# Kernel tuning notes

Measured on AMD Instinct MI355X. Metric: run time of the kernel, lower is better.

## Reference

```python
import jax, jax.numpy as jnp
import numpy as np

BN_EPS = 1e-5
INTERP_EPS = 1e-8


def setup_inputs() -> dict:
    key = jax.random.key(0)
    ks = jax.random.split(key, 8)
    B, N, S, D1, D2 = 8, 8192, 2048, 128, 256
    C_in, C_mid, C_out = D1 + D2, 256, 256
    return {
        "xyz1": jax.random.normal(ks[0], (B, 3, N), dtype=jnp.float32),
        "xyz2": jax.random.normal(ks[1], (B, 3, S), dtype=jnp.float32),
        "points1": jax.random.normal(ks[2], (B, D1, N), dtype=jnp.float32),
        "points2": jax.random.normal(ks[3], (B, D2, S), dtype=jnp.float32),
        "W0": jax.random.normal(ks[4], (C_mid, C_in), dtype=jnp.float32) * (1.0 / np.sqrt(C_in)),
        "b0": jnp.zeros((C_mid,), dtype=jnp.float32),
        "gamma0": jnp.ones((C_mid,), dtype=jnp.float32),
        "beta0": jnp.zeros((C_mid,), dtype=jnp.float32),
        "W1": jax.random.normal(ks[5], (C_out, C_mid), dtype=jnp.float32) * (1.0 / np.sqrt(C_mid)),
        "b1": jnp.zeros((C_out,), dtype=jnp.float32),
    }


def reference(xyz1, xyz2, points1, points2, W0, b0, gamma0, beta0, W1, b1):
    B, _, N = xyz1.shape
    S = xyz2.shape[2]
    x1 = jnp.transpose(xyz1, (0, 2, 1))  # (B, N, 3)
    x2 = jnpp = jnp.transpose(xyz2, (0, 2, 1))  # (B, S, 3)
    # squared distances: (B, N, S)
    d = (jnp.sum(x1 ** 2, -1)[:, :, None]
         + jnp.sum(x2 ** 2, -1)[:, None, :]
         - 2.0 * jnp.einsum('bnc,bsc->bns', x1, x2))
    # 3 nearest neighbors (fused top-3 instead of full sort; same math)
    neg_d, idx = jax.lax.top_k(-d, 3)  # (B, N, 3)
    dists = -neg_d
    recip = 1.0 / (dists + INTERP_EPS)
    weight = recip / jnp.sum(recip, axis=2, keepdims=True)  # (B, N, 3)
    p2t = jnp.transpose(points2, (0, 2, 1))  # (B, S, D2)
    D2 = p2t.shape[-1]
    gathered = jnp.take_along_axis(p2t, idx.reshape(B, N * 3, 1), axis=1).reshape(B, N, 3, D2)
    interp = jnp.einsum('bnkc,bnk->bcn', gathered, weight)  # (B, D2, N)
    new_points = jnp.concatenate([interp, points1], axis=1)  # (B, D2+D1, N)
    # conv0 (1x1) + BatchNorm (train mode, batch stats) + ReLU
    h = jnp.einsum('oc,bcn->bon', W0, new_points) + b0[None, :, None]
    mean = jnp.mean(h, axis=(0, 2), keepdims=True)
    var = jnp.mean((h - mean) ** 2, axis=(0, 2), keepdims=True)  # biased, as torch BN
    h = gamma0[None, :, None] * (h - mean) * jax.lax.rsqrt(var + BN_EPS) + beta0[None, :, None]
    h = jax.nn.relu(h)
    # conv1 (1x1) + Identity (module pairs conv1 with nn.Identity) + ReLU
    h = jnp.einsum('oc,bcn->bon', W1, h) + b1[None, :, None]
    return jax.nn.relu(h)
```

## Files before the change

### kernel.cpp

```cpp
#include <hip/hip_runtime.h>
#include <stdint.h>

constexpr int B = 8, N = 8192, S = 2048, D1 = 128, D2 = 256;
constexpr int CIN = 384, CMID = 256, COUT = 256;

typedef __attribute__((ext_vector_type(8))) _Float16 half8;
typedef __attribute__((ext_vector_type(4))) _Float16 half4;
typedef __attribute__((ext_vector_type(4))) float f32x4;

union HU { uint32_t u; _Float16 h[2]; };


__global__ __launch_bounds__(256) void k_prep(const float* __restrict__ xyz2,
                                              float* __restrict__ dout) {
  const int gid = blockIdx.x * 256 + threadIdx.x;
  const int b = gid >> 11, s = gid & 2047;
  const float* x2 = xyz2 + (size_t)b * 3 * S;
  const float sx = x2[s], sy = x2[s + S], sz = x2[s + 2 * S];
  float4 v = {sx, sy, sz, sx * sx + sy * sy + sz * sz};
  *(float4*)(dout + ((size_t)(b * 256 + 208)) * 8192 + (size_t)s * 4) = v;
}

__global__ __launch_bounds__(256) void k_top3(const float* __restrict__ xyz1,
                                              const float* __restrict__ dP4,
                                              uint32_t* __restrict__ pw3) {
  __shared__ float md[4][3][64];
  __shared__ int mi[4][3][64];
  __shared__ float snrm[64];
  const int tid = threadIdx.x;
  const int wv = tid >> 6, lane = tid & 63;
  const int b = blockIdx.y;
  const int n = blockIdx.x * 64 + lane;
  const float* x1 = xyz1 + (size_t)b * 3 * N;
  const float ax = x1[n], ay = x1[n + N], az = x1[n + 2 * N];
  const float* P4 = dP4 + ((size_t)(b * 256 + 208)) * 8192;
  if (wv == 0) snrm[lane] = ax * ax + ay * ay + az * az;

  const float nax = -2.f * ax, nay = -2.f * ay, naz = -2.f * az;
  float e0 = 1e30f, e1 = 1e30f, e2 = 1e30f;
  int j0 = 0, j1 = 0, j2 = 0;
  const int s0 = wv * (S / 4), s1 = s0 + (S / 4);
#pragma unroll 8
  for (int s = s0; s < s1; ++s) {
    const float4 v = *(const float4*)(P4 + (size_t)s * 4);
    const float d = fmaf(nax, v.x, fmaf(nay, v.y, fmaf(naz, v.z, v.w)));
    const bool c0 = d < e0, c1 = d < e1, c2 = d < e2;
    const int u2 = c1 ? j1 : s;
    const int u1 = c0 ? j0 : s;
    j2 = c2 ? u2 : j2;
    j1 = c1 ? u1 : j1;
    j0 = c0 ? s : j0;
    e2 = __builtin_amdgcn_fmed3f(e1, e2, d);
    e1 = __builtin_amdgcn_fmed3f(e0, e1, d);
    e0 = fminf(e0, d);
  }
  md[wv][0][lane] = e0; mi[wv][0][lane] = j0;
  md[wv][1][lane] = e1; mi[wv][1][lane] = j1;
  md[wv][2][lane] = e2; mi[wv][2][lane] = j2;
  __syncthreads();
  if (tid < 64) {
    float f0 = md[0][0][tid], f1 = md[0][1][tid], f2 = md[0][2][tid];
    int g0 = mi[0][0][tid], g1 = mi[0][1][tid], g2 = mi[0][2][tid];
#pragma unroll
    for (int w = 1; w < 4; ++w)
#pragma unroll
      for (int k = 0; k < 3; ++k) {
        float d = md[w][k][tid];
        int i = mi[w][k][tid];
        if (d < f2) {
          if (d < f1) {
            f2 = f1; g2 = g1;
            if (d < f0) { f1 = f0; g1 = g0; f0 = d; g0 = i; }
            else        { f1 = d;  g1 = i; }
          } else { f2 = d; g2 = i; }
        }
      }
    const float rn = snrm[tid];
    float q0 = fmaxf(f0 + rn, 0.f);
    float q1 = fmaxf(f1 + rn, 0.f);
    float q2 = fmaxf(f2 + rn, 0.f);
    float r0 = 1.0f / (q0 + 1e-8f), r1 = 1.0f / (q1 + 1e-8f), r2 = 1.0f / (q2 + 1e-8f);
    float inv = 1.0f / (r0 + r1 + r2);
    auto pack = [](int i, float w) -> uint32_t {
      uint32_t q = (uint32_t)(w * 2097152.0f + 0.5f);
      if (q > 0x1FFFFFu) q = 0x1FFFFFu;
      return ((uint32_t)i << 21) | q;
    };
    size_t base = ((size_t)b * N + blockIdx.x * 64 + tid) * 3;
    pw3[base]     = pack(g0, r0 * inv);
    pw3[base + 1] = pack(g1, r1 * inv);
    pw3[base + 2] = pack(g2, r2 * inv);
  }
}

__global__ __launch_bounds__(256) void k_G(const float* __restrict__ points2,
                                           const float* __restrict__ W0,
                                           float* __restrict__ dout) {
  __shared__ half8 A_lds[4][256];
  __shared__ half8 B_lds[4][32];
  __shared__ float CT[32][258];
  const int tid = threadIdx.x;
  const int b = blockIdx.x >> 6;
  const int s0 = (blockIdx.x & 63) * 32;
  f32x4 acc[4][2] = {};
  const int wv = tid >> 6, lane = tid & 63;
  const int ln = lane & 15, quad = lane >> 4;
  const int bn = tid & 31, bkc = tid >> 5;
  const int ar = tid >> 3, ac4 = tid & 7;

  for (int kk = 0; kk < 256; kk += 32) {
    __syncthreads();
#pragma unroll
    for (int p = 0; p < 8; ++p) {
      int row = ar + 32 * p;
      const float4 v = *(const float4*)(W0 + (size_t)row * CIN + kk + ac4 * 4);
      half4 hv = {(_Float16)v.x, (_Float16)v.y, (_Float16)v.z, (_Float16)v.w};
      *(half4*)((_Float16*)&A_lds[ac4 >> 1][row] + (ac4 & 1) * 4) = hv;
    }
    {
      half4 hv;
#pragma unroll
      for (int j = 0; j < 4; ++j)
        hv[j] = (_Float16)points2[((size_t)(b * 256 + kk + bkc * 4 + j)) * S + s0 + bn];
      *(half4*)((_Float16*)&B_lds[bkc >> 1][bn] + (bkc & 1) * 4) = hv;
    }
    __syncthreads();
    half8 af[4], bf[2];
#pragma unroll
    for (int i = 0; i < 4; ++i) af[i] = A_lds[quad][wv * 64 + i * 16 + ln];
#pragma unroll
    for (int j = 0; j < 2; ++j) bf[j] = B_lds[quad][j * 16 + ln];
#pragma unroll
    for (int i = 0; i < 4; ++i)
#pragma unroll
      for (int j = 0; j < 2; ++j)
        acc[i][j] = __builtin_amdgcn_mfma_f32_16x16x32_f16(af[i], bf[j], acc[i][j], 0, 0, 0);
  }
  __syncthreads();
#pragma unroll
  for (int i = 0; i < 4; ++i)
#pragma unroll
    for (int reg = 0; reg < 4; ++reg) {
      int row = wv * 64 + i * 16 + quad * 4 + reg;
#pragma unroll
      for (int j = 0; j < 2; ++j) CT[j * 16 + ln][row] = acc[i][j][reg];
    }
  __syncthreads();
  const int sl = tid >> 3, g = tid & 7;
  float* g0 = dout + ((size_t)(b * 256 + 128)) * 8192 + (size_t)(s0 + sl) * 256 + g * 32;
#pragma unroll
  for (int q = 0; q < 8; ++q)
    *(float4*)(g0 + q * 4) = *(const float4*)&CT[sl][g * 32 + q * 4];
}

__global__ __launch_bounds__(256) void k_interp(const uint32_t* __restrict__ pw3,
                                                const float* __restrict__ dout_c,
                                                uint32_t* __restrict__ dout_u) {
  __shared__ int sidx[96];
  __shared__ float sw[96];
  const int tid = threadIdx.x;
  const int b = blockIdx.x >> 8;
  const int n0 = (blockIdx.x & 255) * 32;
  if (tid < 96) {
    uint32_t p = pw3[((size_t)b * N + n0) * 3 + tid];
    sidx[tid] = (int)(p >> 21);
    sw[tid] = (float)(p & 0x1FFFFFu) * (1.0f / 2097152.0f);
  }
  __syncthreads();
  const int colL = tid >> 3, p = tid & 7;
  const float* Gb = dout_c + ((size_t)(b * 256 + 128)) * 8192;
  float a[32];
#pragma unroll
  for (int q = 0; q < 32; ++q) a[q] = 0.f;
#pragma unroll
  for (int k = 0; k < 3; ++k) {
    int j = sidx[colL * 3 + k];
    float w = sw[colL * 3 + k];
    const float* g = Gb + (size_t)j * 256 + p * 32;
#pragma unroll
    for (int q = 0; q < 8; ++q) {
      float4 v = *(const float4*)(g + q * 4);
      a[q * 4 + 0] += w * v.x; a[q * 4 + 1] += w * v.y;
      a[q * 4 + 2] += w * v.z; a[q * 4 + 3] += w * v.w;
    }
  }
#pragma unroll
  for (int q = 0; q < 16; ++q) {
    int cp = p * 16 + q;
    HU u;
    u.h[0] = (_Float16)a[2 * q];
    u.h[1] = (_Float16)a[2 * q + 1];
    dout_u[((size_t)(b * 256 + cp)) * 8192 + n0 + colL] = u.u;
  }
}

__global__ __launch_bounds__(256) void k_wpack(const float* __restrict__ W0,
                                               const float* __restrict__ W1,
                                               _Float16* __restrict__ W1h,
                                               _Float16* __restrict__ W0h) {
  const int bid = blockIdx.x;
  if (bid < 64) {
    const int gid = bid * 256 + threadIdx.x;
    const float4 v = *(const float4*)(W1 + (size_t)gid * 4);
    half4 h = {(_Float16)v.x, (_Float16)v.y, (_Float16)v.z, (_Float16)v.w};
    *(half4*)(W1h + (size_t)gid * 4) = h;
  } else {
    const int gid = (bid - 64) * 256 + threadIdx.x;
    const int row = gid >> 5, c4 = gid & 31;
    const float4 v = *(const float4*)(W0 + (size_t)row * CIN + 256 + c4 * 4);
    half4 h = {(_Float16)v.x, (_Float16)v.y, (_Float16)v.z, (_Float16)v.w};
    *(half4*)(W0h + (size_t)row * 128 + c4 * 4) = h;
  }
}

__global__ __launch_bounds__(256) void k_h(uint32_t* __restrict__ h2,
                                           float* __restrict__ dpart,
                                           const float* __restrict__ points1,
                                           const _Float16* __restrict__ W0h,
                                           const float* __restrict__ b0) {
  __shared__ half8 B_lds[16][32];
  __shared__ float red_s[256], red_q[256], sb0[256];
  const int tid = threadIdx.x;
  const int b = blockIdx.x >> 8;
  const int cb = blockIdx.x & 255;
  const int n0 = cb * 32;
  sb0[tid] = b0[tid];
  const int wv = tid >> 6, lane = tid & 63;
  const int ln = lane & 15, quad = lane >> 4;

  f32x4 acc[4][2];
#pragma unroll
  for (int i = 0; i < 4; ++i) {
    const int rb = wv * 64 + i * 16 + quad * 4;
    const int cp0 = rb >> 1;
#pragma unroll
    for (int j = 0; j < 2; ++j) {
      const int col = n0 + j * 16 + ln;
      const size_t a0 = ((size_t)(b * 256 + cp0)) * 8192 + col;
      HU ua, ub;
      ua.u = h2[a0];
      ub.u = h2[a0 + 8192];
      acc[i][j][0] = (float)ua.h[0];
      acc[i][j][1] = (float)ua.h[1];
      acc[i][j][2] = (float)ub.h[0];
      acc[i][j][3] = (float)ub.h[1];
    }
  }
  {
    const int col = tid & 31;
    const int kc0 = tid >> 5;
#pragma unroll
    for (int it = 0; it < 2; ++it) {
      const int kc = kc0 + 8 * it;
      half8 hv;
#pragma unroll
      for (int j = 0; j < 8; ++j)
        hv[j] = (_Float16)points1[((size_t)(b * D1 + kc * 8 + j)) * N + n0 + col];
      B_lds[kc][col] = hv;
    }
  }
  __syncthreads();
  for (int kk = 0; kk < 128; kk += 32) {
    half8 af[4], bf[2];
#pragma unroll
    for (int i = 0; i < 4; ++i) {
      const int row = wv * 64 + i * 16 + ln;
      af[i] = *(const half8*)(W0h + (size_t)row * 128 + kk + quad * 8);
    }
#pragma unroll
    for (int j = 0; j < 2; ++j)
      bf[j] = B_lds[(kk >> 3) + quad][j * 16 + ln];
#pragma unroll
    for (int i = 0; i < 4; ++i)
#pragma unroll
      for (int j = 0; j < 2; ++j)
        acc[i][j] = __builtin_amdgcn_mfma_f32_16x16x32_f16(af[i], bf[j], acc[i][j], 0, 0, 0);
  }
#pragma unroll
  for (int i = 0; i < 4; ++i) {
    const int rb = wv * 64 + i * 16 + quad * 4;
    const int cp0 = rb >> 1;
    float rs[4] = {0.f, 0.f, 0.f, 0.f}, rq[4] = {0.f, 0.f, 0.f, 0.f};
#pragma unroll
    for (int j = 0; j < 2; ++j) {
      const int col = n0 + j * 16 + ln;
      const size_t a0 = ((size_t)(b * 256 + cp0)) * 8192 + col;
      _Float16 e0 = (_Float16)(acc[i][j][0] + sb0[rb + 0]);
      _Float16 e1 = (_Float16)(acc[i][j][1] + sb0[rb + 1]);
      _Float16 e2 = (_Float16)(acc[i][j][2] + sb0[rb + 2]);
      _Float16 e3 = (_Float16)(acc[i][j][3] + sb0[rb + 3]);
      HU o0, o1;
      o0.h[0] = e0; o0.h[1] = e1; o1.h[0] = e2; o1.h[1] = e3;
      h2[a0] = o0.u;
      h2[a0 + 8192] = o1.u;
      float f0 = (float)e0, f1 = (float)e1, f2 = (float)e2, f3 = (float)e3;
      rs[0] += f0; rq[0] += f0 * f0;
      rs[1] += f1; rq[1] += f1 * f1;
      rs[2] += f2; rq[2] += f2 * f2;
      rs[3] += f3; rq[3] += f3 * f3;
    }
#pragma unroll
    for (int reg = 0; reg < 4; ++reg) {
      float s = rs[reg], q = rq[reg];
#pragma unroll
      for (int m = 1; m < 16; m <<= 1) {
        s += __shfl_xor(s, m);
        q += __shfl_xor(q, m);
      }
      if (ln == 0) { red_s[rb + reg] = s; red_q[rb + reg] = q; }
    }
  }
  __syncthreads();
  float* part = dpart + ((size_t)(b * 256 + 192)) * 8192 + (size_t)cb * 512;
  part[tid] = red_s[tid];
  part[256 + tid] = red_q[tid];
}

__global__ __launch_bounds__(256) void k_bn(const float* __restrict__ dpart,
                                            const float* __restrict__ gamma,
                                            const float* __restrict__ beta,
                                            float* __restrict__ bna,
                                            float* __restrict__ bnb) {
  const int c = blockIdx.x;
  const int tid = threadIdx.x;
  float s = 0.f, q = 0.f;
#pragma unroll
  for (int u = tid; u < 2048; u += 256) {
    int b = u >> 8, cb = u & 255;
    const float* part = dpart + ((size_t)(b * 256 + 192)) * 8192 + (size_t)cb * 512;
    s += part[c];
    q += part[256 + c];
  }
#pragma unroll
  for (int m = 1; m < 64; m <<= 1) {
    s += __shfl_xor(s, m);
    q += __shfl_xor(q, m);
  }
  __shared__ float ls[4], lq[4];
  if ((tid & 63) == 0) { ls[tid >> 6] = s; lq[tid >> 6] = q; }
  __syncthreads();
  if (tid == 0) {
    float st = ls[0] + ls[1] + ls[2] + ls[3];
    float qt = lq[0] + lq[1] + lq[2] + lq[3];
    const float invn = 1.0f / (float)(B * N);
    float mean = st * invn;
    float var = qt * invn - mean * mean;
    float a = gamma[c] * rsqrtf(var + 1e-5f);
    bna[c] = a;
    bnb[c] = beta[c] - mean * a;
  }
}

__global__ __launch_bounds__(256) void k_fused1(const uint32_t* h2,
                                                const _Float16* __restrict__ W1h,
                                                const float* __restrict__ b1,
                                                const float* __restrict__ bna,
                                                const float* __restrict__ bnb,
                                                float* out) {
  __shared__ uint32_t Hh[32 * 33 * 4];
  __shared__ float sa[256], sb[256], sb1[256];
  const int tid = threadIdx.x;
  const int b = blockIdx.x >> 8;
  const int n0 = (blockIdx.x & 255) * 32;
  sa[tid] = bna[tid]; sb[tid] = bnb[tid]; sb1[tid] = b1[tid];
  __syncthreads();
  {
    const int c4 = tid & 7;
    const int rg = tid >> 3;
#pragma unroll
    for (int q = 0; q < 4; ++q) {
      const int cp = rg + 32 * q;
      const uint4 v = *(const uint4*)&h2[((size_t)(b * 256 + cp)) * 8192 + n0 + c4 * 4];
      const int k0 = 2 * cp;
      const float a0 = sa[k0], a1 = sa[k0 + 1], b0v = sb[k0], b1v = sb[k0 + 1];
      const int kc = cp >> 2, sub = cp & 3;
      const uint32_t vv[4] = {v.x, v.y, v.z, v.w};
#pragma unroll
      for (int m = 0; m < 4; ++m) {
        HU u; u.u = vv[m];
        float v0 = a0 * (float)u.h[0] + b0v;
        float v1 = a1 * (float)u.h[1] + b1v;
        HU o;
        o.h[0] = (_Float16)(v0 > 0.f ? v0 : 0.f);
        o.h[1] = (_Float16)(v1 > 0.f ? v1 : 0.f);
        Hh[((kc * 33) + c4 * 4 + m) * 4 + sub] = o.u;
      }
    }
  }
  __syncthreads();
  f32x4 acc[4][2] = {};
  const int wv = tid >> 6, lane = tid & 63;
  const int ln = lane & 15, quad = lane >> 4;
  for (int kk = 0; kk < 256; kk += 32) {
    half8 af[4], bf[2];
#pragma unroll
    for (int i = 0; i < 4; ++i) {
      int row = wv * 64 + i * 16 + ln;
      af[i] = *(const half8*)(W1h + (size_t)row * CMID + kk + quad * 8);
    }
#pragma unroll
    for (int j = 0; j < 2; ++j)
      bf[j] = *(const half8*)&Hh[(((kk >> 3) + quad) * 33 + j * 16 + ln) * 4];
#pragma unroll
    for (int i = 0; i < 4; ++i)
#pragma unroll
      for (int j = 0; j < 2; ++j)
        acc[i][j] = __builtin_amdgcn_mfma_f32_16x16x32_f16(af[i], bf[j], acc[i][j], 0, 0, 0);
  }
#pragma unroll
  for (int i = 0; i < 4; ++i) {
    const int rb = wv * 64 + i * 16 + quad * 4;
#pragma unroll
    for (int reg = 0; reg < 4; ++reg) {
      int row = rb + reg;
      float bias = sb1[row];
      float* orow = out + ((size_t)(b * 256 + row)) * 8192 + n0;
#pragma unroll
      for (int j = 0; j < 2; ++j)
        orow[j * 16 + ln] = fmaxf(acc[i][j][reg] + bias, 0.f);
    }
  }
}

extern "C" void kernel_launch(void* const* d_in, const int* in_sizes, int n_in,
                              void* d_out, int out_size, void* d_ws, size_t ws_size,
                              hipStream_t stream) {
  const float* xyz1 = (const float*)d_in[0];
  const float* xyz2 = (const float*)d_in[1];
  const float* points1 = (const float*)d_in[2];
  const float* points2 = (const float*)d_in[3];
  const float* W0 = (const float*)d_in[4];
  const float* b0 = (const float*)d_in[5];
  const float* gamma0 = (const float*)d_in[6];
  const float* beta0 = (const float*)d_in[7];
  const float* W1 = (const float*)d_in[8];
  const float* b1 = (const float*)d_in[9];
  float* out = (float*)d_out;

  char* ws = (char*)d_ws;
  float* bna = (float*)ws;
  float* bnb = (float*)(ws + 1024);
  uint32_t* pw3 = (uint32_t*)(ws + 2048);
  _Float16* W1h = (_Float16*)(ws + 2048);
  _Float16* W0h = (_Float16*)(ws + 2048 + 131072);

  k_prep<<<dim3(B * S / 256), 256, 0, stream>>>(xyz2, out);
  k_top3<<<dim3(N / 64, B), 256, 0, stream>>>(xyz1, out, pw3);
  k_G<<<dim3(B * 64), 256, 0, stream>>>(points2, W0, out);
  k_interp<<<dim3(B * N / 32), 256, 0, stream>>>(pw3, out, (uint32_t*)out);
  k_wpack<<<dim3(96), 256, 0, stream>>>(W0, W1, W1h, W0h);
  k_h<<<dim3(B * N / 32), 256, 0, stream>>>((uint32_t*)out, out, points1, W0h, b0);
  k_bn<<<dim3(256), 256, 0, stream>>>(out, gamma0, beta0, bna, bnb);
  k_fused1<<<dim3(B * N / 32), 256, 0, stream>>>((const uint32_t*)out, W1h, b1,
                                                 bna, bnb, out);
}
```

Measured before the change: 332.5 us.

## Split top-3 search over S into four chunks with LDS-staged points and merge kernel

```diff
diff --git a/kernel.cpp b/kernel.cpp
--- a/kernel.cpp
+++ b/kernel.cpp
@@ -11,39 +11,38 @@
 union HU { uint32_t u; _Float16 h[2]; };
 
 
-__global__ __launch_bounds__(256) void k_prep(const float* __restrict__ xyz2,
-                                              float* __restrict__ dout) {
-  const int gid = blockIdx.x * 256 + threadIdx.x;
-  const int b = gid >> 11, s = gid & 2047;
-  const float* x2 = xyz2 + (size_t)b * 3 * S;
-  const float sx = x2[s], sy = x2[s + S], sz = x2[s + 2 * S];
-  float4 v = {sx, sy, sz, sx * sx + sy * sy + sz * sz};
-  *(float4*)(dout + ((size_t)(b * 256 + 208)) * 8192 + (size_t)s * 4) = v;
-}
-
-__global__ __launch_bounds__(256) void k_top3(const float* __restrict__ xyz1,
-                                              const float* __restrict__ dP4,
-                                              uint32_t* __restrict__ pw3) {
+__global__ __launch_bounds__(256) void k_top3a(const float* __restrict__ xyz1,
+                                               const float* __restrict__ xyz2,
+                                               float* __restrict__ dout) {
+  __shared__ float4 Pq[512];
   __shared__ float md[4][3][64];
   __shared__ int mi[4][3][64];
-  __shared__ float snrm[64];
   const int tid = threadIdx.x;
   const int wv = tid >> 6, lane = tid & 63;
   const int b = blockIdx.y;
+  const int sp = blockIdx.z;
+  const int sbase = sp * 512;
   const int n = blockIdx.x * 64 + lane;
   const float* x1 = xyz1 + (size_t)b * 3 * N;
+  const float* x2 = xyz2 + (size_t)b * 3 * S;
+
+  for (int j = tid; j < 512; j += 256) {
+    const int s = sbase + j;
+    float sx = x2[s], sy = x2[s + S], sz = x2[s + 2 * S];
+    Pq[j] = float4{sx, sy, sz, sx * sx + sy * sy + sz * sz};
+  }
   const float ax = x1[n], ay = x1[n + N], az = x1[n + 2 * N];
-  const float* P4 = dP4 + ((size_t)(b * 256 + 208)) * 8192;
-  if (wv == 0) snrm[lane] = ax * ax + ay * ay + az * az;
-
   const float nax = -2.f * ax, nay = -2.f * ay, naz = -2.f * az;
+  __syncthreads();
+
   float e0 = 1e30f, e1 = 1e30f, e2 = 1e30f;
   int j0 = 0, j1 = 0, j2 = 0;
-  const int s0 = wv * (S / 4), s1 = s0 + (S / 4);
+  const int q0 = wv * 128, q1 = q0 + 128;
 #pragma unroll 8
-  for (int s = s0; s < s1; ++s) {
-    const float4 v = *(const float4*)(P4 + (size_t)s * 4);
+  for (int j = q0; j < q1; ++j) {
+    const float4 v = Pq[j];
     const float d = fmaf(nax, v.x, fmaf(nay, v.y, fmaf(naz, v.z, v.w)));
+    const int s = sbase + j;
     const bool c0 = d < e0, c1 = d < e1, c2 = d < e2;
     const int u2 = c1 ? j1 : s;
     const int u1 = c0 ? j0 : s;
@@ -75,22 +74,53 @@
           } else { f2 = d; g2 = i; }
         }
       }
-    const float rn = snrm[tid];
-    float q0 = fmaxf(f0 + rn, 0.f);
-    float q1 = fmaxf(f1 + rn, 0.f);
-    float q2 = fmaxf(f2 + rn, 0.f);
-    float r0 = 1.0f / (q0 + 1e-8f), r1 = 1.0f / (q1 + 1e-8f), r2 = 1.0f / (q2 + 1e-8f);
-    float inv = 1.0f / (r0 + r1 + r2);
-    auto pack = [](int i, float w) -> uint32_t {
-      uint32_t q = (uint32_t)(w * 2097152.0f + 0.5f);
-      if (q > 0x1FFFFFu) q = 0x1FFFFFu;
-      return ((uint32_t)i << 21) | q;
-    };
-    size_t base = ((size_t)b * N + blockIdx.x * 64 + tid) * 3;
-    pw3[base]     = pack(g0, r0 * inv);
-    pw3[base + 1] = pack(g1, r1 * inv);
-    pw3[base + 2] = pack(g2, r2 * inv);
-  }
+    const int nm = blockIdx.x * 64 + tid;
+    float* cd = dout + ((size_t)(b * 256 + 128)) * 8192;
+    uint32_t* ci = (uint32_t*)cd + 98304;
+    cd[(sp * 3 + 0) * N + nm] = f0; ci[(sp * 3 + 0) * N + nm] = (uint32_t)g0;
+    cd[(sp * 3 + 1) * N + nm] = f1; ci[(sp * 3 + 1) * N + nm] = (uint32_t)g1;
+    cd[(sp * 3 + 2) * N + nm] = f2; ci[(sp * 3 + 2) * N + nm] = (uint32_t)g2;
+  }
+}
+
+__global__ __launch_bounds__(256) void k_top3b(const float* __restrict__ xyz1,
+                                               const float* __restrict__ dout,
+                                               uint32_t* __restrict__ pw3) {
+  const int gid = blockIdx.x * 256 + threadIdx.x;
+  const int b = gid >> 13, n = gid & 8191;
+  const float* cd = dout + ((size_t)(b * 256 + 128)) * 8192;
+  const uint32_t* ci = (const uint32_t*)cd + 98304;
+  float f0 = 1e30f, f1 = 1e30f, f2 = 1e30f;
+  int g0 = 0, g1 = 0, g2 = 0;
+#pragma unroll
+  for (int t = 0; t < 12; ++t) {
+    float d = cd[(size_t)t * N + n];
+    int i = (int)ci[(size_t)t * N + n];
+    if (d < f2) {
+      if (d < f1) {
+        f2 = f1; g2 = g1;
+        if (d < f0) { f1 = f0; g1 = g0; f0 = d; g0 = i; }
+        else        { f1 = d;  g1 = i; }
+      } else { f2 = d; g2 = i; }
+    }
+  }
+  const float* x1 = xyz1 + (size_t)b * 3 * N;
+  const float ax = x1[n], ay = x1[n + N], az = x1[n + 2 * N];
+  const float rn = ax * ax + ay * ay + az * az;
+  float q0 = fmaxf(f0 + rn, 0.f);
+  float q1 = fmaxf(f1 + rn, 0.f);
+  float q2 = fmaxf(f2 + rn, 0.f);
+  float r0 = 1.0f / (q0 + 1e-8f), r1 = 1.0f / (q1 + 1e-8f), r2 = 1.0f / (q2 + 1e-8f);
+  float inv = 1.0f / (r0 + r1 + r2);
+  auto pack = [](int i, float w) -> uint32_t {
+    uint32_t q = (uint32_t)(w * 2097152.0f + 0.5f);
+    if (q > 0x1FFFFFu) q = 0x1FFFFFu;
+    return ((uint32_t)i << 21) | q;
+  };
+  size_t base = ((size_t)b * N + n) * 3;
+  pw3[base]     = pack(g0, r0 * inv);
+  pw3[base + 1] = pack(g1, r1 * inv);
+  pw3[base + 2] = pack(g2, r2 * inv);
 }
 
 __global__ __launch_bounds__(256) void k_G(const float* __restrict__ points2,
@@ -444,8 +474,8 @@
   _Float16* W1h = (_Float16*)(ws + 2048);
   _Float16* W0h = (_Float16*)(ws + 2048 + 131072);
 
-  k_prep<<<dim3(B * S / 256), 256, 0, stream>>>(xyz2, out);
-  k_top3<<<dim3(N / 64, B), 256, 0, stream>>>(xyz1, out, pw3);
+  k_top3a<<<dim3(N / 64, B, 4), 256, 0, stream>>>(xyz1, xyz2, out);
+  k_top3b<<<dim3(B * N / 256), 256, 0, stream>>>(xyz1, out, pw3);
   k_G<<<dim3(B * 64), 256, 0, stream>>>(points2, W0, out);
   k_interp<<<dim3(B * N / 32), 256, 0, stream>>>(pw3, out, (uint32_t*)out);
   k_wpack<<<dim3(96), 256, 0, stream>>>(W0, W1, W1h, W0h);
```

New measurement: 309.8 us. -6.8%, faster.
